# Optimization experiments

Hardware: AMD Instinct MI355X
Metric: run time of the kernel (lower is better)

Reference implementation:

```python
import jax, jax.numpy as jnp
import numpy as np

N, R, A, F, T, O = 50000, 5, 8, 128, 2, 128
RADIUS = 1.0

def _template_vertices():
    # polar grid of template vertices in cartesian coords, shape (R, A, 2)
    radii = (np.arange(1, R + 1) / R) * RADIUS
    angles = np.linspace(0.0, 2.0 * np.pi, A, endpoint=False)
    x = radii[:, None] * np.cos(angles)[None, :]
    y = radii[:, None] * np.sin(angles)[None, :]
    return np.stack([x, y], axis=-1)

def _interp_coeffs():
    # Gaussian interpolation coefficients (concrete define_interpolation_coefficients),
    # shape (R, A, R*A), rows normalized -- constant, non-trainable (built in build()).
    v = _template_vertices().reshape(R * A, 2)
    d2 = ((v[:, None, :] - v[None, :, :]) ** 2).sum(-1)
    sigma = RADIUS / R
    w = np.exp(-d2 / (2.0 * sigma ** 2))
    w = w / w.sum(axis=1, keepdims=True)
    return w.reshape(R, A, R * A).astype(np.float32)

def setup_inputs() -> dict:
    key = jax.random.key(0)
    k1, k2, k3, k4, k5 = jax.random.split(key, 5)
    mesh_signal = jax.random.normal(k1, (N, F), dtype=jnp.float32)
    bary_w = jax.random.uniform(k2, (N, R, A, 3), dtype=jnp.float32)
    bary_w = bary_w / bary_w.sum(axis=-1, keepdims=True)  # barycentric weights sum to 1
    bary_idx = jax.random.randint(k3, (N, R, A, 3), 0, N, dtype=jnp.int32)
    glorot = lambda k, shp: jax.random.uniform(
        k, shp, jnp.float32, -1.0, 1.0) * np.sqrt(6.0 / (shp[-1] + shp[-2]))
    template_weights = glorot(k4, (A, T, O, F))  # (n_angular, templates, out, feat)
    bias = glorot(k5, (T, O))
    return {"mesh_signal": mesh_signal, "bary_w": bary_w,
            "template_weights": template_weights, "bias": bias,
            "interp_coeffs": jnp.asarray(_interp_coeffs()),
            "bary_idx": bary_idx}

def reference(mesh_signal, bary_w, template_weights, bias, interp_coeffs, bary_idx):
    # --- patch operator: barycentric gather + interpolation ---
    gathered = mesh_signal[bary_idx]                       # (N,R,A,3,F) irregular gather
    interp = (bary_w[..., None] * gathered).sum(axis=-2)   # (N,R,A,F)
    # prior: mix all R*A template-vertex signals per output template vertex
    sig = interp.reshape(-1, R * A, F)                     # (N,RA,F)
    interp = jnp.einsum('nkf,rak->nraf', sig, interp_coeffs)  # (N,R,A,F)
    # --- fold: all A rotations (rotation_delta=1), vectorized by rolling weights ---
    rots = jnp.arange(0, A, 1)                             # K = A rotations
    idx = (jnp.arange(A)[None, :] + rots[:, None]) % A     # (K,A): roll(interp,+r) == roll(W,-r)
    W_all = template_weights[idx]                          # (K,A,T,O,F)
    # TF adds bias before summing over (R,A) axes -> bias appears R*A times
    z = jnp.einsum('nraf,katof->nkto', interp, W_all) + (R * A) * bias  # (N,K,T,O)
    out = jax.nn.relu(z).sum(axis=2)                       # sum over templates -> (N,K,O)
    return out
```

## Files before the change

kernel.cpp:

```cpp
#include <hip/hip_runtime.h>
#include <hip/hip_bf16.h>
#include <stdint.h>

#define NN 50000
#define RR 5
#define AA 8
#define FF 128
#define TT 2
#define OO 128
#define KDIM 1024
#define KB 512
#define RA 40

typedef __attribute__((ext_vector_type(8))) short short8;
typedef __attribute__((ext_vector_type(4))) float f32x4;
typedef __attribute__((ext_vector_type(2))) float f32x2;
typedef __attribute__((ext_vector_type(4))) int i32x4;
typedef __attribute__((ext_vector_type(2))) unsigned u32x2;

#if __has_builtin(__builtin_elementwise_fma)
__device__ inline f32x2 pk_fma(f32x2 a, f32x2 b, f32x2 c) {
  return __builtin_elementwise_fma(a, b, c);
}
#else
__device__ inline f32x2 pk_fma(f32x2 a, f32x2 b, f32x2 c) {
  f32x2 d;
  asm("v_pk_fma_f32 %0, %1, %2, %3" : "=v"(d) : "v"(a), "v"(b), "v"(c));
  return d;
}
#endif

__device__ inline void gload_lds16(const void* g, void* l) {
  __builtin_amdgcn_global_load_lds(
      (const __attribute__((address_space(1))) unsigned int*)g,
      (__attribute__((address_space(3))) unsigned int*)l, 16, 0, 0);
}

__global__ void prep_kernel(const float* __restrict__ mesh,
                            const float* __restrict__ coeffs,
                            const float* __restrict__ W,
                            const float* __restrict__ bary_w,
                            const int* __restrict__ bary_idx,
                            __hip_bfloat16* __restrict__ meshq,
                            float* __restrict__ G,
                            __hip_bfloat16* __restrict__ Bh,
                            unsigned* __restrict__ packb,
                            int do_pack) {
  int tid = blockIdx.x * blockDim.x + threadIdx.x;
  int stride = gridDim.x * blockDim.x;
  for (int i = tid; i < NN * FF; i += stride) {
    int n = i >> 7, f = i & 127;
    int p = f >> 5, fo = f & 31;
    meshq[((long)p * NN + n) * 32 + fo] = __float2bfloat16(mesh[i]);
  }
  for (int i = tid; i < AA * RA; i += stride) {
    int p = i / RA, k = i % RA;
    int a = p & 3;
    float s1 = 0.f, s2 = 0.f;
    for (int r = 0; r < RR; ++r) {
      s1 += coeffs[(r * AA + a) * RA + k];
      s2 += coeffs[(r * AA + a + 4) * RA + k];
    }
    G[i] = (p < 4) ? (s1 + s2) : (s1 - s2);
  }
  for (int i = tid; i < 2048 * KB; i += stride) {
    int col = i >> 9, k = i & 511;
    int half = col >> 10, c = col & 1023;
    int o = c >> 3, t = (c >> 2) & 1, j = c & 3;
    int a4 = k >> 7, f = k & 127;
    int m = (a4 + j) & 3;
    float w0 = W[((m * TT + t) * OO + o) * FF + f];
    float w4 = W[(((m + 4) * TT + t) * OO + o) * FF + f];
    float v;
    if (half == 0) v = 0.5f * (w0 + w4);
    else {
      v = 0.5f * (w0 - w4);
      if (a4 + j >= 4) v = -v;
    }
    Bh[i] = __float2bfloat16(v);
  }
  if (do_pack) {
    for (int i = tid; i < NN * 120; i += stride) {
      __hip_bfloat16 h = __float2bfloat16(bary_w[i]);
      unsigned wb = *(unsigned short*)&h;
      packb[i] = ((unsigned)bary_idx[i] << 16) | wb;
    }
  }
}

__global__ __launch_bounds__(256) void s_pass_packed(
    const __hip_bfloat16* __restrict__ meshq,
    const unsigned* __restrict__ packb,
    const float* __restrict__ G,
    __hip_bfloat16* __restrict__ Sout,
    int p) {
  __shared__ unsigned pk_s[32 * 120];
  __shared__ float g_s[AA * RA];
  int tid = threadIdx.x;
  long n0 = (long)blockIdx.x * 32;
  int nnode = (NN - n0 < 32) ? (int)(NN - n0) : 32;
  int nvec = nnode * 30;
  const i32x4* psrc = (const i32x4*)(packb + n0 * 120);
  for (int i = tid; i < nvec; i += 256) {
    i32x4 v = __builtin_nontemporal_load(psrc + i);
    ((i32x4*)pk_s)[i] = v;
  }
  for (int i = tid; i < AA * RA; i += 256) g_s[i] = G[i];
  __syncthreads();

  int g = tid >> 3;
  int fo = tid & 7;
  long n = n0 + g;
  if (n >= NN) return;
  const unsigned* pg = pk_s + g * 120;
  const char* mbase = (const char*)meshq + (long)p * NN * 64 + fo * 8;

  f32x2 accA[AA], accB[AA];
#pragma unroll
  for (int a = 0; a < AA; ++a) {
    accA[a] = (f32x2){0.f, 0.f};
    accB[a] = (f32x2){0.f, 0.f};
  }

#pragma unroll 2
  for (int k = 0; k < RA; ++k) {
    f32x2 sA = (f32x2){0.f, 0.f}, sB = (f32x2){0.f, 0.f};
#pragma unroll
    for (int j = 0; j < 3; ++j) {
      unsigned v = pg[k * 3 + j];
      long row = v >> 16;
      float w = __uint_as_float(v << 16);
      f32x2 wv = (f32x2){w, w};
      u32x2 u = *(const u32x2*)(mbase + row * 64);
      f32x2 lo = (f32x2){__uint_as_float(u[0] << 16),
                         __uint_as_float(u[0] & 0xffff0000u)};
      f32x2 hi = (f32x2){__uint_as_float(u[1] << 16),
                         __uint_as_float(u[1] & 0xffff0000u)};
      sA = pk_fma(wv, lo, sA);
      sB = pk_fma(wv, hi, sB);
    }
#pragma unroll
    for (int a = 0; a < AA; ++a) {
      float cc = g_s[a * RA + k];
      f32x2 cv = (f32x2){cc, cc};
      accA[a] = pk_fma(cv, sA, accA[a]);
      accB[a] = pk_fma(cv, sB, accB[a]);
    }
  }

  long base = n * KDIM + p * 32 + fo * 4;
#pragma unroll
  for (int a = 0; a < AA; ++a) {
    __hip_bfloat16 h0 = __float2bfloat16(accA[a][0]);
    __hip_bfloat16 h1 = __float2bfloat16(accA[a][1]);
    __hip_bfloat16 h2 = __float2bfloat16(accB[a][0]);
    __hip_bfloat16 h3 = __float2bfloat16(accB[a][1]);
    unsigned w0 = (unsigned)*(unsigned short*)&h0 |
                  ((unsigned)*(unsigned short*)&h1 << 16);
    unsigned w1 = (unsigned)*(unsigned short*)&h2 |
                  ((unsigned)*(unsigned short*)&h3 << 16);
    u32x2 st = (u32x2){w0, w1};
    __builtin_nontemporal_store(st, (u32x2*)(Sout + base + a * FF));
  }
}

__global__ __launch_bounds__(256) void s_pass_kernel(
    const __hip_bfloat16* __restrict__ meshq,
    const float* __restrict__ bary_w,
    const int* __restrict__ bary_idx,
    const float* __restrict__ G,
    __hip_bfloat16* __restrict__ Sout,
    int p) {
  __shared__ float w_s[16 * 120];
  __shared__ int i_s[16 * 120];
  __shared__ float g_s[AA * RA];
  int tid = threadIdx.x;
  long n0 = (long)blockIdx.x * 16;
  const f32x4* wsrc = (const f32x4*)(bary_w + n0 * 120);
  const i32x4* isrc = (const i32x4*)(bary_idx + n0 * 120);
  for (int i = tid; i < 480; i += 256) {
    f32x4 wv = __builtin_nontemporal_load(wsrc + i);
    ((f32x4*)w_s)[i] = wv;
    i32x4 iv = __builtin_nontemporal_load(isrc + i);
    ((i32x4*)i_s)[i] = iv;
  }
  for (int i = tid; i < AA * RA; i += 256) g_s[i] = G[i];
  __syncthreads();
  int g = tid >> 4;
  int fo = tid & 15;
  long n = n0 + g;
  const float* wg = w_s + g * 120;
  const int* ig = i_s + g * 120;
  const char* mbase = (const char*)meshq + (long)p * NN * 64 + fo * 4;
  float sx_acc[AA], sy_acc[AA];
#pragma unroll
  for (int a = 0; a < AA; ++a) { sx_acc[a] = 0.f; sy_acc[a] = 0.f; }
#pragma unroll 2
  for (int k = 0; k < RA; ++k) {
    float sx = 0.f, sy = 0.f;
#pragma unroll
    for (int j = 0; j < 3; ++j) {
      int row = ig[k * 3 + j];
      unsigned u = *(const unsigned*)(mbase + (long)row * 64);
      float w = wg[k * 3 + j];
      sx += w * __uint_as_float(u << 16);
      sy += w * __uint_as_float(u & 0xffff0000u);
    }
#pragma unroll
    for (int a = 0; a < AA; ++a) {
      float c = g_s[a * RA + k];
      sx_acc[a] += c * sx;
      sy_acc[a] += c * sy;
    }
  }
  long base = n * KDIM + p * 32 + fo * 2;
#pragma unroll
  for (int a = 0; a < AA; ++a) {
    __hip_bfloat16 hx = __float2bfloat16(sx_acc[a]);
    __hip_bfloat16 hy = __float2bfloat16(sy_acc[a]);
    unsigned u = (unsigned)*(unsigned short*)&hx | ((unsigned)*(unsigned short*)&hy << 16);
    __builtin_nontemporal_store(u, (unsigned*)(Sout + base + a * FF));
  }
}

__global__ __launch_bounds__(256, 2) void gemm_kernel(
    const __hip_bfloat16* __restrict__ Sh,
    const __hip_bfloat16* __restrict__ Bh,
    const float* __restrict__ bias,
    float* __restrict__ out) {
  int bx = blockIdx.x;
  int by = blockIdx.y;
  int cb = by & 7;
  int mt = ((by >> 3) << 3) + bx;
  if (mt >= 391) return;
  int row0 = mt * 128;
  int cE0 = cb * 128;

  int tid = threadIdx.x;
  int lane = tid & 63;
  int wid = tid >> 6;
  int wave_m = wid >> 1;
  int wave_n = wid & 1;

  __shared__ __align__(16) char lds[79872];

  long srcSp[2], srcB[2];
  int dstA[2], dstBd[2];
#pragma unroll
  for (int i = 0; i < 2; ++i) {
    int li = i * 256 + tid;
    int r = li >> 2, sp = li & 3;
    int sl = sp ^ ((r >> 1) & 3);
    int rowA = row0 + r;
    if (rowA >= NN) rowA = NN - 1;
    srcSp[i] = (long)rowA * KDIM + sl * 8;
    dstA[i] = li * 16;
    srcB[i] = (long)(cE0 + r) * KB + sl * 8;
    dstBd[i] = 16384 + li * 16;
  }
  int offA[4], offB[4];
#pragma unroll
  for (int m = 0; m < 4; ++m) {
    int r = wave_m * 64 + m * 16 + (lane & 15);
    int phys = (lane >> 4) ^ ((r >> 1) & 3);
    offA[m] = r * 64 + phys * 16;
  }
#pragma unroll
  for (int n = 0; n < 4; ++n) {
    int c = wave_n * 64 + n * 16 + (lane & 15);
    int phys = (lane >> 4) ^ ((c >> 1) & 3);
    offB[n] = 16384 + c * 64 + phys * 16;
  }

  f32x4 acc[4][8];
#pragma unroll
  for (int m = 0; m < 4; ++m)
#pragma unroll
    for (int q = 0; q < 8; ++q) acc[m][q] = (f32x4){0.f, 0.f, 0.f, 0.f};

#define STAGE(T)                                                              \
  {                                                                           \
    char* base_ = lds + ((T) & 1) * 32768;                                    \
    long k0_ = (long)(T) * 32;                                                \
    _Pragma("unroll") for (int i_ = 0; i_ < 2; ++i_)                          \
        gload_lds16(Sh + srcSp[i_] + k0_, base_ + dstA[i_]);                  \
    _Pragma("unroll") for (int i_ = 0; i_ < 2; ++i_)                          \
        gload_lds16(Sh + srcSp[i_] + 512 + k0_, base_ + 8192 + dstA[i_]);     \
    _Pragma("unroll") for (int i_ = 0; i_ < 2; ++i_)                          \
        gload_lds16(Bh + srcB[i_] + k0_, base_ + dstBd[i_]);                  \
    _Pragma("unroll") for (int i_ = 0; i_ < 2; ++i_)                          \
        gload_lds16(Bh + srcB[i_] + (long)1024 * KB + k0_,                    \
                    base_ + 8192 + dstBd[i_]);                                \
  }

#define GSTEP(STP, DOSTAGE)                                                   \
  {                                                                           \
    const char* cbuf = lds + ((STP) & 1) * 32768;                             \
    asm volatile("s_waitcnt vmcnt(0)" ::: "memory");                          \
    __builtin_amdgcn_sched_barrier(0);                                        \
    __builtin_amdgcn_s_barrier();                                             \
    __builtin_amdgcn_sched_barrier(0);                                        \
    if (DOSTAGE) STAGE((STP) + 1)                                             \
    __builtin_amdgcn_sched_barrier(0);                                        \
    short8 aE[4], aO[4], bE[4], bO[4];                                        \
    _Pragma("unroll") for (int m_ = 0; m_ < 4; ++m_) {                        \
      aE[m_] = *(const short8*)(cbuf + offA[m_]);                             \
      aO[m_] = *(const short8*)(cbuf + offA[m_] + 8192);                      \
    }                                                                         \
    _Pragma("unroll") for (int n_ = 0; n_ < 4; ++n_) {                        \
      bE[n_] = *(const short8*)(cbuf + offB[n_]);                             \
      bO[n_] = *(const short8*)(cbuf + offB[n_] + 8192);                      \
    }                                                                         \
    __builtin_amdgcn_s_setprio(1);                                            \
    _Pragma("unroll") for (int m_ = 0; m_ < 4; ++m_)                          \
        _Pragma("unroll") for (int n_ = 0; n_ < 4; ++n_) {                    \
      acc[m_][n_] = __builtin_amdgcn_mfma_f32_16x16x32_bf16(                  \
          aE[m_], bE[n_], acc[m_][n_], 0, 0, 0);                              \
      acc[m_][n_ + 4] = __builtin_amdgcn_mfma_f32_16x16x32_bf16(              \
          aO[m_], bO[n_], acc[m_][n_ + 4], 0, 0, 0);                          \
    }                                                                         \
    __builtin_amdgcn_s_setprio(0);                                            \
    __builtin_amdgcn_sched_barrier(0);                                        \
  }

  STAGE(0)
  GSTEP(0, 1)  GSTEP(1, 1)  GSTEP(2, 1)  GSTEP(3, 1)
  GSTEP(4, 1)  GSTEP(5, 1)  GSTEP(6, 1)  GSTEP(7, 1)
  GSTEP(8, 1)  GSTEP(9, 1)  GSTEP(10, 1) GSTEP(11, 1)
  GSTEP(12, 1) GSTEP(13, 1) GSTEP(14, 1) GSTEP(15, 0)

  __syncthreads();
  float* lout = (float*)lds;
  int c = lane & 15;
  int t = (c >> 2) & 1;
  int j = c & 3;
  int hi = lane >> 4;
  float bq[4];
#pragma unroll
  for (int n = 0; n < 4; ++n) {
    int o_l = wave_n * 8 + n * 2 + (c >> 3);
    bq[n] = 40.f * bias[t * OO + cb * 16 + o_l];
  }
#pragma unroll
  for (int m = 0; m < 4; ++m) {
#pragma unroll
    for (int n = 0; n < 4; ++n) {
      int o_l = wave_n * 8 + n * 2 + (c >> 3);
#pragma unroll
      for (int i = 0; i < 4; ++i) {
        float zE = acc[m][n][i];
        float zO = acc[m][n + 4][i];
        float rlo = fmaxf(zE + zO + bq[n], 0.f);
        float rhi = fmaxf(zE - zO + bq[n], 0.f);
        rlo += __shfl_xor(rlo, 4);
        rhi += __shfl_xor(rhi, 4);
        if (!(lane & 4)) {
          int node = wave_m * 64 + m * 16 + hi * 4 + i;
          lout[node * 156 + j * 20 + o_l] = rlo;
          lout[node * 156 + (j + 4) * 20 + o_l] = rhi;
        }
      }
    }
  }
  __syncthreads();

#pragma unroll
  for (int it = 0; it < 16; ++it) {
    int gi = it * 256 + tid;
    int node = gi >> 5;
    int rem = gi & 31;
    int kr = rem >> 2, o4 = rem & 3;
    int grow = row0 + node;
    if (grow < NN) {
      f32x4 v = *(const f32x4*)(lout + node * 156 + kr * 20 + o4 * 4);
      long gaddr = (long)grow * 1024 + kr * 128 + cb * 16 + o4 * 4;
      __builtin_nontemporal_store(v, (f32x4*)(out + gaddr));
    }
  }
}

extern "C" void kernel_launch(void* const* d_in, const int* in_sizes, int n_in,
                              void* d_out, int out_size, void* d_ws, size_t ws_size,
                              hipStream_t stream) {
  const float* mesh   = (const float*)d_in[0];
  const float* bary_w = (const float*)d_in[1];
  const float* W      = (const float*)d_in[2];
  const float* bias   = (const float*)d_in[3];
  const float* coeffs = (const float*)d_in[4];
  const int* bidx     = (const int*)d_in[5];
  float* out = (float*)d_out;
  char* ws = (char*)d_ws;

  __hip_bfloat16* meshq = (__hip_bfloat16*)ws;
  float* G              = (float*)(ws + 12800000);
  __hip_bfloat16* Bh    = (__hip_bfloat16*)(ws + 12801280);
  __hip_bfloat16* Smat  = (__hip_bfloat16*)(ws + 16995584);
  unsigned* packb       = (unsigned*)(ws + 119395584);

  int do_pack = (ws_size >= 143395584UL) ? 1 : 0;

  prep_kernel<<<dim3(2048), dim3(256), 0, stream>>>(mesh, coeffs, W, bary_w, bidx,
                                                    meshq, G, Bh, packb, do_pack);
  if (do_pack) {
    for (int p = 0; p < 4; ++p)
      s_pass_packed<<<dim3(1563), dim3(256), 0, stream>>>(meshq, packb, G, Smat, p);
  } else {
    for (int p = 0; p < 4; ++p)
      s_pass_kernel<<<dim3(3125), dim3(256), 0, stream>>>(meshq, bary_w, bidx, G, Smat, p);
  }
  gemm_kernel<<<dim3(8, 392), dim3(256), 0, stream>>>(Smat, Bh, bias, out);
}
```

Measured before the change: 375.6 us.

## Pre-swizzle B into MFMA fragment layout and load it directly from global

The prep kernel now writes the weight matrix B in a layout that already matches per-lane MFMA operands, ordered by column group, k-step and lane. The GEMM kernel then reads B fragments straight from global memory (L2-resident) into registers each k-step, so only the A tile is staged through LDS and the LDS double buffer shrinks. This removes B's LDS staging and LDS reads, at the cost of global-load latency sitting on the MFMA critical path, since the B loads are issued right after the barrier with no prefetch.

```diff
diff --git a/kernel.cpp b/kernel.cpp
--- a/kernel.cpp
+++ b/kernel.cpp
@@ -43,7 +43,7 @@
                             const int* __restrict__ bary_idx,
                             __hip_bfloat16* __restrict__ meshq,
                             float* __restrict__ G,
-                            __hip_bfloat16* __restrict__ Bh,
+                            __hip_bfloat16* __restrict__ B2,
                             unsigned* __restrict__ packb,
                             int do_pack) {
   int tid = blockIdx.x * blockDim.x + threadIdx.x;
@@ -63,9 +63,14 @@
     }
     G[i] = (p < 4) ? (s1 + s2) : (s1 - s2);
   }
-  for (int i = tid; i < 2048 * KB; i += stride) {
-    int col = i >> 9, k = i & 511;
-    int half = col >> 10, c = col & 1023;
+  for (int e = tid; e < 2048 * KB; e += stride) {
+    int sub = e & 7;
+    int lane = (e >> 3) & 63;
+    int kt = (e >> 9) & 15;
+    int cg = (e >> 13) & 63;
+    int half = e >> 19;
+    int c = cg * 16 + (lane & 15);
+    int k = kt * 32 + (lane >> 4) * 8 + sub;
     int o = c >> 3, t = (c >> 2) & 1, j = c & 3;
     int a4 = k >> 7, f = k & 127;
     int m = (a4 + j) & 3;
@@ -77,7 +82,7 @@
       v = 0.5f * (w0 - w4);
       if (a4 + j >= 4) v = -v;
     }
-    Bh[i] = __float2bfloat16(v);
+    B2[e] = __float2bfloat16(v);
   }
   if (do_pack) {
     for (int i = tid; i < NN * 120; i += stride) {
@@ -225,7 +230,7 @@
 
 __global__ __launch_bounds__(256, 2) void gemm_kernel(
     const __hip_bfloat16* __restrict__ Sh,
-    const __hip_bfloat16* __restrict__ Bh,
+    const __hip_bfloat16* __restrict__ B2,
     const float* __restrict__ bias,
     float* __restrict__ out) {
   int bx = blockIdx.x;
@@ -234,7 +239,6 @@
   int mt = ((by >> 3) << 3) + bx;
   if (mt >= 391) return;
   int row0 = mt * 128;
-  int cE0 = cb * 128;
 
   int tid = threadIdx.x;
   int lane = tid & 63;
@@ -244,8 +248,8 @@
 
   __shared__ __align__(16) char lds[79872];
 
-  long srcSp[2], srcB[2];
-  int dstA[2], dstBd[2];
+  long srcSp[2];
+  int dstA[2];
 #pragma unroll
   for (int i = 0; i < 2; ++i) {
     int li = i * 256 + tid;
@@ -255,21 +259,21 @@
     if (rowA >= NN) rowA = NN - 1;
     srcSp[i] = (long)rowA * KDIM + sl * 8;
     dstA[i] = li * 16;
-    srcB[i] = (long)(cE0 + r) * KB + sl * 8;
-    dstBd[i] = 16384 + li * 16;
-  }
-  int offA[4], offB[4];
+  }
+  int offA[4];
 #pragma unroll
   for (int m = 0; m < 4; ++m) {
     int r = wave_m * 64 + m * 16 + (lane & 15);
     int phys = (lane >> 4) ^ ((r >> 1) & 3);
     offA[m] = r * 64 + phys * 16;
   }
+  const char* b2c = (const char*)B2;
+  long bOffE[4], bOffO[4];
 #pragma unroll
   for (int n = 0; n < 4; ++n) {
-    int c = wave_n * 64 + n * 16 + (lane & 15);
-    int phys = (lane >> 4) ^ ((c >> 1) & 3);
-    offB[n] = 16384 + c * 64 + phys * 16;
+    int cg = cb * 8 + wave_n * 4 + n;
+    bOffE[n] = ((long)cg * 16) * 1024 + lane * 16;
+    bOffO[n] = bOffE[n] + (long)64 * 16 * 1024;
   }
 
   f32x4 acc[4][8];
@@ -280,36 +284,32 @@
 
 #define STAGE(T)                                                              \
   {                                                                           \
-    char* base_ = lds + ((T) & 1) * 32768;                                    \
+    char* base_ = lds + ((T) & 1) * 16384;                                    \
     long k0_ = (long)(T) * 32;                                                \
     _Pragma("unroll") for (int i_ = 0; i_ < 2; ++i_)                          \
         gload_lds16(Sh + srcSp[i_] + k0_, base_ + dstA[i_]);                  \
     _Pragma("unroll") for (int i_ = 0; i_ < 2; ++i_)                          \
         gload_lds16(Sh + srcSp[i_] + 512 + k0_, base_ + 8192 + dstA[i_]);     \
-    _Pragma("unroll") for (int i_ = 0; i_ < 2; ++i_)                          \
-        gload_lds16(Bh + srcB[i_] + k0_, base_ + dstBd[i_]);                  \
-    _Pragma("unroll") for (int i_ = 0; i_ < 2; ++i_)                          \
-        gload_lds16(Bh + srcB[i_] + (long)1024 * KB + k0_,                    \
-                    base_ + 8192 + dstBd[i_]);                                \
   }
 
 #define GSTEP(STP, DOSTAGE)                                                   \
   {                                                                           \
-    const char* cbuf = lds + ((STP) & 1) * 32768;                             \
+    const char* cbuf = lds + ((STP) & 1) * 16384;                             \
     asm volatile("s_waitcnt vmcnt(0)" ::: "memory");                          \
     __builtin_amdgcn_sched_barrier(0);                                        \
     __builtin_amdgcn_s_barrier();                                             \
     __builtin_amdgcn_sched_barrier(0);                                        \
+    short8 bE[4], bO[4];                                                      \
+    _Pragma("unroll") for (int n_ = 0; n_ < 4; ++n_) {                        \
+      bE[n_] = *(const short8*)(b2c + bOffE[n_] + (long)(STP) * 1024);        \
+      bO[n_] = *(const short8*)(b2c + bOffO[n_] + (long)(STP) * 1024);        \
+    }                                                                         \
     if (DOSTAGE) STAGE((STP) + 1)                                             \
     __builtin_amdgcn_sched_barrier(0);                                        \
-    short8 aE[4], aO[4], bE[4], bO[4];                                        \
+    short8 aE[4], aO[4];                                                      \
     _Pragma("unroll") for (int m_ = 0; m_ < 4; ++m_) {                        \
       aE[m_] = *(const short8*)(cbuf + offA[m_]);                             \
       aO[m_] = *(const short8*)(cbuf + offA[m_] + 8192);                      \
-    }                                                                         \
-    _Pragma("unroll") for (int n_ = 0; n_ < 4; ++n_) {                        \
-      bE[n_] = *(const short8*)(cbuf + offB[n_]);                             \
-      bO[n_] = *(const short8*)(cbuf + offB[n_] + 8192);                      \
     }                                                                         \
     __builtin_amdgcn_s_setprio(1);                                            \
     _Pragma("unroll") for (int m_ = 0; m_ < 4; ++m_)                          \
@@ -393,14 +393,14 @@
 
   __hip_bfloat16* meshq = (__hip_bfloat16*)ws;
   float* G              = (float*)(ws + 12800000);
-  __hip_bfloat16* Bh    = (__hip_bfloat16*)(ws + 12801280);
+  __hip_bfloat16* B2    = (__hip_bfloat16*)(ws + 12801280);
   __hip_bfloat16* Smat  = (__hip_bfloat16*)(ws + 16995584);
   unsigned* packb       = (unsigned*)(ws + 119395584);
 
   int do_pack = (ws_size >= 143395584UL) ? 1 : 0;
 
   prep_kernel<<<dim3(2048), dim3(256), 0, stream>>>(mesh, coeffs, W, bary_w, bidx,
-                                                    meshq, G, Bh, packb, do_pack);
+                                                    meshq, G, B2, packb, do_pack);
   if (do_pack) {
     for (int p = 0; p < 4; ++p)
       s_pass_packed<<<dim3(1563), dim3(256), 0, stream>>>(meshq, packb, G, Smat, p);
@@ -408,5 +408,5 @@
     for (int p = 0; p < 4; ++p)
       s_pass_kernel<<<dim3(3125), dim3(256), 0, stream>>>(meshq, bary_w, bidx, G, Smat, p);
   }
-  gemm_kernel<<<dim3(8, 392), dim3(256), 0, stream>>>(Smat, Bh, bias, out);
-}
+  gemm_kernel<<<dim3(8, 392), dim3(256), 0, stream>>>(Smat, B2, bias, out);
+}
```

After: 381.7 us. No clear change (+1.6%).
